# Kernel optimization log

Hardware: AMD Instinct MI355X
Metric: run time of the kernel (lower is better)

The kernel has to match this reference:

```python
import jax, jax.numpy as jnp
import numpy as np

IN_F, OUT_F, GROUP = 4096, 11008, 128

# NF4 codebook (normalized-float-4 levels), matches NF4_LEVELS in the source
NF4_LEVELS = jnp.array([
    -1.0, -0.6961928009986877, -0.5250730514526367, -0.39491748809814453,
    -0.28444138169288635, -0.18477343022823334, -0.09105003625154495, 0.0,
    0.07958029955625534, 0.16093020141124725, 0.24611230194568634,
    0.33791524171829224, 0.44070982933044434, 0.5626170039176941,
    0.7229568362236023, 1.0], dtype=jnp.float32)


def setup_inputs() -> dict:
    key = jax.random.key(0)
    k0, k1, k2, k3 = jax.random.split(key, 4)
    x = jax.random.normal(k0, (32, 1, IN_F), dtype=jnp.float32)
    # one int32 per packed byte; low nibble = even element code, high nibble = odd
    packed = jax.random.randint(k1, (OUT_F * IN_F // 2,), 0, 256, dtype=jnp.int32)
    # per-group absmax scales (positive)
    scales = jax.random.uniform(k2, (OUT_F * IN_F // GROUP,), dtype=jnp.float32) * 0.02 + 1e-4
    bias_param = jax.random.normal(k3, (OUT_F,), dtype=jnp.float32)
    return {"x": x, "packed": packed, "scales": scales, "bias_param": bias_param}


def dequant_nf4(packed, scales):
    # unpack two 4-bit codes per byte; interleave as quantized[0::2]=low, [1::2]=high
    low = packed & 15
    high = (packed >> 4) & 15
    codes = jnp.stack([low, high], axis=-1).reshape(-1)          # [OUT_F*IN_F]
    vals = NF4_LEVELS[codes]                                      # codebook lookup
    w = (vals.reshape(-1, GROUP) * scales[:, None]).reshape(OUT_F, IN_F)
    return w


def reference(x, packed, scales, bias_param):
    W = dequant_nf4(packed, scales)                               # [OUT_F, IN_F]
    # y = x @ W^T + b  (F.linear semantics)
    return jnp.einsum('bsi,oi->bso', x, W) + bias_param
```

## Files before the change

kernel.cpp:

```cpp
#include <hip/hip_runtime.h>
#include <hip/hip_bf16.h>

#define IN_F   4096
#define OUT_F  11008
#define BATCH  32
#define NTILE  64
#define KSPLIT 8
#define GRID_N (OUT_F / NTILE)

typedef __attribute__((ext_vector_type(8))) short  bf16x8;
typedef __attribute__((ext_vector_type(4))) float  f32x4;
typedef __attribute__((ext_vector_type(4))) int    i32x4;
typedef __attribute__((ext_vector_type(4))) float  float4v;

static __device__ __constant__ float NF4_LEVELS[16] = {
    -1.0f, -0.6961928009986877f, -0.5250730514526367f, -0.39491748809814453f,
    -0.28444138169288635f, -0.18477343022823334f, -0.09105003625154495f, 0.0f,
    0.07958029955625534f, 0.16093020141124725f, 0.24611230194568634f,
    0.33791524171829224f, 0.44070982933044434f, 0.5626170039176941f,
    0.7229568362236023f, 1.0f};

__global__ void prelude_kernel(const float* __restrict__ x,
                               const float* __restrict__ bias,
                               unsigned short* __restrict__ frag,
                               float* __restrict__ out) {
    const int bid = blockIdx.x, tid = threadIdx.x;
    if (bid < 64) {
        int T  = bid * 256 + tid;
        int st = T >> 13;
        int kb = (T >> 6) & 127;
        int l  = T & 63;
        int row = st * 16 + (l & 15);
        int k0  = kb * 32 + (l >> 4) * 8;
        const float* src = x + (size_t)row * IN_F + k0;
        unsigned w[4];
        #pragma unroll
        for (int e = 0; e < 4; ++e) {
            unsigned lo = __builtin_bit_cast(unsigned short, __float2bfloat16(src[2 * e]));
            unsigned hi = __builtin_bit_cast(unsigned short, __float2bfloat16(src[2 * e + 1]));
            w[e] = lo | (hi << 16);
        }
        i32x4 v = { (int)w[0], (int)w[1], (int)w[2], (int)w[3] };
        *reinterpret_cast<i32x4*>(frag + ((size_t)st * 8192 + kb * 64 + l) * 8) = v;
    } else {
        int t2 = (bid - 64) * 256 + tid;
        int i  = t2 * 4;
        int o  = i % OUT_F;
        float4v b = *reinterpret_cast<const float4v*>(bias + o);
        *reinterpret_cast<float4v*>(out + i) = b;
    }
}

__global__ __launch_bounds__(256, 4) void nf4_gemm_kernel(
        const int* __restrict__ packed,
        const float* __restrict__ scales,
        const unsigned short* __restrict__ frag,
        float* __restrict__ out)
{
    __shared__ unsigned lds[5120];

    const int tid  = threadIdx.x;
    const int wave = tid >> 6;
    const int lane = tid & 63;
    const int col  = lane & 15;
    const int g    = lane >> 4;

    const int n0      = blockIdx.x * NTILE;
    const int by      = blockIdx.y;
    const int rowbase = n0 + wave * 16;

    #pragma unroll
    for (int q = 0; q < 4; ++q) {
        int e = q * 64 + lane;
        unsigned lo = __builtin_bit_cast(unsigned short, __float2bfloat16(NF4_LEVELS[e & 15]));
        unsigned hi = __builtin_bit_cast(unsigned short, __float2bfloat16(NF4_LEVELS[(e >> 4) & 15]));
        lds[wave * 256 + e] = lo | (hi << 16);
    }

    float4v scv = *reinterpret_cast<const float4v*>(
        scales + (size_t)(rowbase + col) * 32 + by * 4);
    float sca[4] = { scv.x, scv.y, scv.z, scv.w };

    const int dperm = (lane & 0x30) | ((lane & 3) << 2) | ((lane >> 2) & 3);
    unsigned* cbuf = &lds[1024 + wave * 1024];

    #define SLOAD(r0, sr)                                                      \
        _Pragma("unroll")                                                      \
        for (int ii = 0; ii < 8; ++ii) {                                       \
            sr[ii] = *reinterpret_cast<const i32x4*>(                          \
                packed + (size_t)(rowbase + (r0) + ii) * (IN_F / 2)            \
                       + by * 256 + lane * 4);                                 \
        }

    #define SWRITE(r0, sr)                                                     \
        _Pragma("unroll")                                                      \
        for (int ii = 0; ii < 8; ++ii) {                                       \
            int rl = (r0) + ii;                                                \
            unsigned v = ((unsigned)(sr[ii][0] & 255))                         \
                       | ((unsigned)(sr[ii][1] & 255) << 8)                    \
                       | ((unsigned)(sr[ii][2] & 255) << 16)                   \
                       | ((unsigned)sr[ii][3] << 24);                          \
            cbuf[(rl * 64 + dperm) ^ ((rl & 7) << 2)] = v;                     \
        }

    {
        i32x4 sr[8];
        SLOAD(0, sr) SWRITE(0, sr)
        SLOAD(8, sr) SWRITE(8, sr)
    }

    f32x4 acc0 = (f32x4){0.f,0.f,0.f,0.f};
    f32x4 acc1 = (f32x4){0.f,0.f,0.f,0.f};

    const unsigned short* f0 = frag;
    const unsigned short* f1 = frag + 65536;

    #pragma unroll
    for (int grp = 0; grp < 4; ++grp) {
        bf16x8 A0[4], A1[4];
        #pragma unroll
        for (int t = 0; t < 4; ++t) {
            int kb = by * 16 + grp * 4 + t;
            A0[t] = *reinterpret_cast<const bf16x8*>(f0 + ((size_t)kb * 64 + lane) * 8);
            A1[t] = *reinterpret_cast<const bf16x8*>(f1 + ((size_t)kb * 64 + lane) * 8);
        }
        i32x4 cd = *reinterpret_cast<const i32x4*>(
            &cbuf[(col * 64 + grp * 16 + g * 4) ^ ((col & 7) << 2)]);

        f32x4 t0 = (f32x4){0.f,0.f,0.f,0.f};
        f32x4 t1 = (f32x4){0.f,0.f,0.f,0.f};
        #pragma unroll
        for (int t = 0; t < 4; ++t) {
            unsigned code = (unsigned)cd[t];
            i32x4 bu;
            bu[0] = (int)lds[wave * 256 + (code & 255u)];
            bu[1] = (int)lds[wave * 256 + ((code >> 8) & 255u)];
            bu[2] = (int)lds[wave * 256 + ((code >> 16) & 255u)];
            bu[3] = (int)lds[wave * 256 + (code >> 24)];
            bf16x8 bf = __builtin_bit_cast(bf16x8, bu);
            t0 = __builtin_amdgcn_mfma_f32_16x16x32_bf16(A0[t], bf, t0, 0, 0, 0);
            t1 = __builtin_amdgcn_mfma_f32_16x16x32_bf16(A1[t], bf, t1, 0, 0, 0);
        }
        #pragma unroll
        for (int j = 0; j < 4; ++j) {
            acc0[j] = fmaf(sca[grp], t0[j], acc0[j]);
            acc1[j] = fmaf(sca[grp], t1[j], acc1[j]);
        }
    }

    #pragma unroll
    for (int j = 0; j < 4; ++j) {
        unsafeAtomicAdd(out + (size_t)(g * 4 + j) * OUT_F + rowbase + col, acc0[j]);
        unsafeAtomicAdd(out + (size_t)(16 + g * 4 + j) * OUT_F + rowbase + col, acc1[j]);
    }
}

extern "C" void kernel_launch(void* const* d_in, const int* in_sizes, int n_in,
                              void* d_out, int out_size, void* d_ws, size_t ws_size,
                              hipStream_t stream) {
    const float* x      = (const float*)d_in[0];
    const int*   packed = (const int*)d_in[1];
    const float* scales = (const float*)d_in[2];
    const float* bias   = (const float*)d_in[3];
    float* out = (float*)d_out;

    unsigned short* frag = (unsigned short*)d_ws;

    prelude_kernel<<<408, 256, 0, stream>>>(x, bias, frag, out);
    nf4_gemm_kernel<<<dim3(GRID_N, KSPLIT), 256, 0, stream>>>(packed, scales, frag, out);
}
```

Baseline: 31.27 us.

## Split K across waves with in-block reduction and async global-to-LDS double buffering

Each block now covers 16 output columns, and its four waves split the K dimension among themselves. The old design spread K across grid.y blocks and combined them with global atomics. Packed weights are streamed straight into LDS through global_load_lds with double buffering, so the register-staged byte repacking is gone. Partial sums are reduced in LDS and written together with the bias, which removes the bias prefill pass and the atomics. The cost is a larger LDS footprint, per-wave vmcnt(0) waits, and four times the code-lookup loads, since each byte now arrives in its own int32.

```diff
diff --git a/kernel.cpp b/kernel.cpp
--- a/kernel.cpp
+++ b/kernel.cpp
@@ -4,8 +4,7 @@
 #define IN_F   4096
 #define OUT_F  11008
 #define BATCH  32
-#define NTILE  64
-#define KSPLIT 8
+#define NTILE  16
 #define GRID_N (OUT_F / NTILE)
 
 typedef __attribute__((ext_vector_type(8))) short  bf16x8;
@@ -21,43 +20,33 @@
     0.7229568362236023f, 1.0f};
 
 __global__ void prelude_kernel(const float* __restrict__ x,
-                               const float* __restrict__ bias,
-                               unsigned short* __restrict__ frag,
-                               float* __restrict__ out) {
-    const int bid = blockIdx.x, tid = threadIdx.x;
-    if (bid < 64) {
-        int T  = bid * 256 + tid;
-        int st = T >> 13;
-        int kb = (T >> 6) & 127;
-        int l  = T & 63;
-        int row = st * 16 + (l & 15);
-        int k0  = kb * 32 + (l >> 4) * 8;
-        const float* src = x + (size_t)row * IN_F + k0;
-        unsigned w[4];
-        #pragma unroll
-        for (int e = 0; e < 4; ++e) {
-            unsigned lo = __builtin_bit_cast(unsigned short, __float2bfloat16(src[2 * e]));
-            unsigned hi = __builtin_bit_cast(unsigned short, __float2bfloat16(src[2 * e + 1]));
-            w[e] = lo | (hi << 16);
-        }
-        i32x4 v = { (int)w[0], (int)w[1], (int)w[2], (int)w[3] };
-        *reinterpret_cast<i32x4*>(frag + ((size_t)st * 8192 + kb * 64 + l) * 8) = v;
-    } else {
-        int t2 = (bid - 64) * 256 + tid;
-        int i  = t2 * 4;
-        int o  = i % OUT_F;
-        float4v b = *reinterpret_cast<const float4v*>(bias + o);
-        *reinterpret_cast<float4v*>(out + i) = b;
+                               unsigned short* __restrict__ frag) {
+    int T  = blockIdx.x * 256 + threadIdx.x;
+    int st = T >> 13;
+    int kb = (T >> 6) & 127;
+    int l  = T & 63;
+    int row = st * 16 + (l & 15);
+    int k0  = kb * 32 + (l >> 4) * 8;
+    const float* src = x + (size_t)row * IN_F + k0;
+    unsigned w[4];
+    #pragma unroll
+    for (int e = 0; e < 4; ++e) {
+        unsigned lo = __builtin_bit_cast(unsigned short, __float2bfloat16(src[2 * e]));
+        unsigned hi = __builtin_bit_cast(unsigned short, __float2bfloat16(src[2 * e + 1]));
+        w[e] = lo | (hi << 16);
     }
+    i32x4 v = { (int)w[0], (int)w[1], (int)w[2], (int)w[3] };
+    *reinterpret_cast<i32x4*>(frag + ((size_t)st * 8192 + kb * 64 + l) * 8) = v;
 }
 
 __global__ __launch_bounds__(256, 4) void nf4_gemm_kernel(
         const int* __restrict__ packed,
         const float* __restrict__ scales,
+        const float* __restrict__ bias,
         const unsigned short* __restrict__ frag,
         float* __restrict__ out)
 {
-    __shared__ unsigned lds[5120];
+    __shared__ unsigned lds[9216];
 
     const int tid  = threadIdx.x;
     const int wave = tid >> 6;
@@ -65,9 +54,7 @@
     const int col  = lane & 15;
     const int g    = lane >> 4;
 
-    const int n0      = blockIdx.x * NTILE;
-    const int by      = blockIdx.y;
-    const int rowbase = n0 + wave * 16;
+    const int n0 = blockIdx.x * NTILE;
 
     #pragma unroll
     for (int q = 0; q < 4; ++q) {
@@ -77,37 +64,31 @@
         lds[wave * 256 + e] = lo | (hi << 16);
     }
 
-    float4v scv = *reinterpret_cast<const float4v*>(
-        scales + (size_t)(rowbase + col) * 32 + by * 4);
-    float sca[4] = { scv.x, scv.y, scv.z, scv.w };
+    float scw[8];
+    {
+        const float* sp = scales + (size_t)(n0 + col) * 32 + wave * 8;
+        float4v sv0 = *reinterpret_cast<const float4v*>(sp);
+        float4v sv1 = *reinterpret_cast<const float4v*>(sp + 4);
+        scw[0]=sv0.x; scw[1]=sv0.y; scw[2]=sv0.z; scw[3]=sv0.w;
+        scw[4]=sv1.x; scw[5]=sv1.y; scw[6]=sv1.z; scw[7]=sv1.w;
+    }
 
-    const int dperm = (lane & 0x30) | ((lane & 3) << 2) | ((lane >> 2) & 3);
-    unsigned* cbuf = &lds[1024 + wave * 1024];
+    unsigned* cbase = &lds[1024 + wave * 2048];
 
-    #define SLOAD(r0, sr)                                                      \
+    #define STAGE(u)                                                           \
         _Pragma("unroll")                                                      \
-        for (int ii = 0; ii < 8; ++ii) {                                       \
-            sr[ii] = *reinterpret_cast<const i32x4*>(                          \
-                packed + (size_t)(rowbase + (r0) + ii) * (IN_F / 2)            \
-                       + by * 256 + lane * 4);                                 \
+        for (int q = 0; q < 4; ++q) {                                          \
+            int rl = q * 4 + (lane >> 4);                                      \
+            int gq = lane & 15;                                                \
+            const int* srcp = packed                                           \
+                + (size_t)(n0 + rl) * (IN_F / 2)                               \
+                + wave * 512 + (u) * 64 + (gq ^ (rl & 7)) * 4;                 \
+            __builtin_amdgcn_global_load_lds(                                  \
+                (const __attribute__((address_space(1))) unsigned int*)srcp,   \
+                (__attribute__((address_space(3))) unsigned int*)              \
+                    (cbase + ((u) & 1) * 1024 + q * 256),                      \
+                16, 0, 0);                                                     \
         }
-
-    #define SWRITE(r0, sr)                                                     \
-        _Pragma("unroll")                                                      \
-        for (int ii = 0; ii < 8; ++ii) {                                       \
-            int rl = (r0) + ii;                                                \
-            unsigned v = ((unsigned)(sr[ii][0] & 255))                         \
-                       | ((unsigned)(sr[ii][1] & 255) << 8)                    \
-                       | ((unsigned)(sr[ii][2] & 255) << 16)                   \
-                       | ((unsigned)sr[ii][3] << 24);                          \
-            cbuf[(rl * 64 + dperm) ^ ((rl & 7) << 2)] = v;                     \
-        }
-
-    {
-        i32x4 sr[8];
-        SLOAD(0, sr) SWRITE(0, sr)
-        SLOAD(8, sr) SWRITE(8, sr)
-    }
 
     f32x4 acc0 = (f32x4){0.f,0.f,0.f,0.f};
     f32x4 acc1 = (f32x4){0.f,0.f,0.f,0.f};
@@ -115,43 +96,67 @@
     const unsigned short* f0 = frag;
     const unsigned short* f1 = frag + 65536;
 
+    STAGE(0)
+
     #pragma unroll
-    for (int grp = 0; grp < 4; ++grp) {
+    for (int u = 0; u < 8; ++u) {
+        asm volatile("s_waitcnt vmcnt(0)" ::: "memory");
+        __builtin_amdgcn_sched_barrier(0);
+        if (u + 1 < 8) { STAGE(u + 1) }
+
         bf16x8 A0[4], A1[4];
         #pragma unroll
         for (int t = 0; t < 4; ++t) {
-            int kb = by * 16 + grp * 4 + t;
+            int kb = wave * 32 + u * 4 + t;
             A0[t] = *reinterpret_cast<const bf16x8*>(f0 + ((size_t)kb * 64 + lane) * 8);
             A1[t] = *reinterpret_cast<const bf16x8*>(f1 + ((size_t)kb * 64 + lane) * 8);
         }
-        i32x4 cd = *reinterpret_cast<const i32x4*>(
-            &cbuf[(col * 64 + grp * 16 + g * 4) ^ ((col & 7) << 2)]);
 
         f32x4 t0 = (f32x4){0.f,0.f,0.f,0.f};
         f32x4 t1 = (f32x4){0.f,0.f,0.f,0.f};
         #pragma unroll
         for (int t = 0; t < 4; ++t) {
-            unsigned code = (unsigned)cd[t];
+            i32x4 cd = *reinterpret_cast<const i32x4*>(
+                &cbase[(u & 1) * 1024 + col * 64 + (((t * 4 + g) ^ (col & 7)) * 4)]);
             i32x4 bu;
-            bu[0] = (int)lds[wave * 256 + (code & 255u)];
-            bu[1] = (int)lds[wave * 256 + ((code >> 8) & 255u)];
-            bu[2] = (int)lds[wave * 256 + ((code >> 16) & 255u)];
-            bu[3] = (int)lds[wave * 256 + (code >> 24)];
+            bu[0] = (int)lds[wave * 256 + ((unsigned)cd[0] & 255u)];
+            bu[1] = (int)lds[wave * 256 + ((unsigned)cd[1] & 255u)];
+            bu[2] = (int)lds[wave * 256 + ((unsigned)cd[2] & 255u)];
+            bu[3] = (int)lds[wave * 256 + ((unsigned)cd[3] & 255u)];
             bf16x8 bf = __builtin_bit_cast(bf16x8, bu);
             t0 = __builtin_amdgcn_mfma_f32_16x16x32_bf16(A0[t], bf, t0, 0, 0, 0);
             t1 = __builtin_amdgcn_mfma_f32_16x16x32_bf16(A1[t], bf, t1, 0, 0, 0);
         }
+        const float sc = scw[u];
         #pragma unroll
         for (int j = 0; j < 4; ++j) {
-            acc0[j] = fmaf(sca[grp], t0[j], acc0[j]);
-            acc1[j] = fmaf(sca[grp], t1[j], acc1[j]);
+            acc0[j] = fmaf(sc, t0[j], acc0[j]);
+            acc1[j] = fmaf(sc, t1[j], acc1[j]);
         }
     }
 
+    float* red = (float*)cbase;
     #pragma unroll
     for (int j = 0; j < 4; ++j) {
-        unsafeAtomicAdd(out + (size_t)(g * 4 + j) * OUT_F + rowbase + col, acc0[j]);
-        unsafeAtomicAdd(out + (size_t)(16 + g * 4 + j) * OUT_F + rowbase + col, acc1[j]);
+        red[(0 * 4 + j) * 64 + g * 16 + col] = acc0[j];
+        red[(1 * 4 + j) * 64 + g * 16 + col] = acc1[j];
+    }
+    __syncthreads();
+
+    #pragma unroll
+    for (int p = 0; p < 2; ++p) {
+        int idx = p * 256 + tid;
+        int b   = idx >> 4;
+        int c   = idx & 15;
+        int h   = b >> 4;
+        int r   = b & 15;
+        int j   = r & 3;
+        int g2  = r >> 2;
+        int slot = (h * 4 + j) * 64 + g2 * 16 + c;
+        const float* rbase = (const float*)&lds[1024];
+        float s = rbase[slot] + rbase[2048 + slot]
+                + rbase[4096 + slot] + rbase[6144 + slot];
+        out[(size_t)b * OUT_F + n0 + c] = s + bias[n0 + c];
     }
 }
 
@@ -166,6 +171,6 @@
 
     unsigned short* frag = (unsigned short*)d_ws;
 
-    prelude_kernel<<<408, 256, 0, stream>>>(x, bias, frag, out);
-    nf4_gemm_kernel<<<dim3(GRID_N, KSPLIT), 256, 0, stream>>>(packed, scales, frag, out);
+    prelude_kernel<<<64, 256, 0, stream>>>(x, frag);
+    nf4_gemm_kernel<<<GRID_N, 256, 0, stream>>>(packed, scales, bias, frag, out);
 }
```

Result: faster. 26.57 us, median of 3 (-15.0%).
